# Kernel optimization log

Measured on AMD Instinct MI355X. Metric: run time of the kernel, lower is better.

The kernel has to match this reference:

```python
import jax, jax.numpy as jnp
import numpy as np

EPS = 1e-12  # F.normalize eps


def setup_inputs() -> dict:
    key = jax.random.key(0)
    ks = jax.random.split(key, 6)
    B, T, D = 8, 4096, 1024
    L, K, CD = 8, 1024, 16
    return {
        "z_e": jax.random.normal(ks[0], (B, T, D), jnp.float32),
        "Wd": jax.random.normal(ks[1], (L, CD, D), jnp.float32) * 0.02,
        "bd": jnp.zeros((L, CD), jnp.float32),
        "cb": jax.random.normal(ks[2], (L, K, CD), jnp.float32) * 0.02,
        "Wu": jax.random.normal(ks[3], (L, D, CD), jnp.float32) * 0.02,
        "bu": jnp.zeros((L, D), jnp.float32),
    }


def _l2norm(x):
    return x / jnp.maximum(jnp.linalg.norm(x, axis=-1, keepdims=True), EPS)


def reference(z_e, Wd, bd, cb, Wu, bu):
    """z_e: (B,T,D). Returns (z_q_concat, codes, commitment_loss, codebook_loss, entropy_loss)."""
    B, T, D = z_e.shape
    L, K, CD = cb.shape
    sg = jax.lax.stop_gradient
    residual = z_e
    zq_list, codes_list = [], []
    commit = jnp.asarray(0.0, z_e.dtype)
    cbl = jnp.asarray(0.0, z_e.dtype)
    for i in range(L):
        # proj_down: Linear(D -> CD), weight (CD, D)
        z_i = jnp.einsum('btd,cd->btc', residual, Wd[i]) + bd[i]  # (B,T,CD)
        flat = z_i.reshape(-1, CD)                                 # (N,CD)
        cb_i = cb[i]                                               # (K,CD)
        # L2-normalized lookup; argmin of euclidean cdist == argmin of squared dist
        zn, cbn = _l2norm(flat), _l2norm(cb_i)
        d2 = (jnp.sum(zn * zn, -1, keepdims=True)
              - 2.0 * (zn @ cbn.T)
              + jnp.sum(cbn * cbn, -1))                            # (N,K)
        codes = jnp.argmin(d2, axis=-1)                            # (N,)
        z_q = cb_i[codes].reshape(B, T, CD)                        # gather from RAW codebook
        commit = commit + jnp.mean((z_i - sg(z_q)) ** 2)
        cbl = cbl + jnp.mean((z_q - sg(z_i)) ** 2)
        zq_list.append(z_i + sg(z_q - z_i))                        # straight-through
        # residual update uses detached z_q; proj_up weight (D, CD)
        residual = residual - (jnp.einsum('btc,dc->btd', sg(z_q), Wu[i]) + bu[i])
        codes_list.append(codes.reshape(B, T))
    z_q_concat = jnp.concatenate(zq_list, axis=-1)                 # (B,T,L*CD)
    codes_all = jnp.stack(codes_list, axis=-1)                     # (B,T,L)
    entropy_loss = jnp.asarray(0.0, z_e.dtype)                     # entropy_loss_weight == 0
    return z_q_concat, codes_all, commit, cbl, entropy_loss
```

## Files before the change

### kernel.cpp

```cpp
#include <hip/hip_runtime.h>
#include <math.h>


#define TAU 3e-4f

#define WS_WACC   0
#define WS_HV64   64
#define WS_G64    2048
#define WS_CBN64  133120
#define WS_CBN32  1247232
#define WS_G32    1902592
#define WS_HV32   1968128
#define WS_BMAT   1968640
#define WS_SBU    2492928

__device__ __forceinline__ void gload_lds16(const void* g, void* l) {
    __builtin_amdgcn_global_load_lds(
        (const __attribute__((address_space(1))) void*)g,
        (__attribute__((address_space(3))) void*)l, 16, 0, 0);
}

__global__ void __launch_bounds__(256) rvq_prep1(
    const float* __restrict__ cb, const float* __restrict__ Wd,
    const float* __restrict__ bu,
    double* __restrict__ cbn64, float* __restrict__ cbn32,
    float* __restrict__ Bmat, double* __restrict__ sbu,
    double* __restrict__ wacc)
{
    const int b = blockIdx.x, t = threadIdx.x;
    if (b < 32) {
        const int idx = b * 256 + t;
        const float* cp = cb + (size_t)idx * 16;
        double v[16]; double n = 0.0;
#pragma unroll
        for (int c = 0; c < 16; ++c) { v[c] = (double)cp[c]; n = fma(v[c], v[c], n); }
        const double iv = 1.0 / fmax(sqrt(n), 1e-12);
        double* r64 = cbn64 + (size_t)idx * 17;
        float*  r32 = cbn32 + (size_t)idx * 20;
        double c2 = 0.0;
#pragma unroll
        for (int c = 0; c < 16; ++c) {
            const double x = v[c] * iv;
            c2 = fma(x, x, c2);
            r64[c] = x; r32[c] = (float)x;
        }
        r64[16] = c2;
        r32[16] = (float)c2; r32[17] = 0.f; r32[18] = 0.f; r32[19] = 0.f;
    } else if (b < 160) {
        const int ic = b - 32;
        const int d0 = t * 4;
        const float4 v = *(const float4*)(Wd + (size_t)ic * 1024 + d0);
        Bmat[(size_t)(d0 + 0) * 128 + ic] = v.x;
        Bmat[(size_t)(d0 + 1) * 128 + ic] = v.y;
        Bmat[(size_t)(d0 + 2) * 128 + ic] = v.z;
        Bmat[(size_t)(d0 + 3) * 128 + ic] = v.w;
    } else if (b < 192) {
        const int idx = b - 160;
        const int i = idx >> 2, d = (idx & 3) * 256 + t;
        double s = 0.0;
        for (int j = 0; j < i; ++j) s += (double)bu[j * 1024 + d];
        sbu[i * 1024 + d] = s;
    } else {
        if (t == 0) wacc[0] = 0.0;
    }
}

__global__ void __launch_bounds__(256) rvq_prep2(
    const float* __restrict__ Wu, const float* __restrict__ Wd,
    const float* __restrict__ bd, const double* __restrict__ sbu,
    double* __restrict__ G64, float* __restrict__ G32,
    double* __restrict__ hv64, float* __restrict__ hv32)
{
    __shared__ double sm2[1200];
    float* smf = (float*)sm2;
    const int b = blockIdx.x, t = threadIdx.x;
    if (b < 64) {
        const int j = b >> 3, i = b & 7;
        if (j >= i) return;
        float* Aus = smf;
        float* Bds = smf + 1280;
        const int a = t >> 4, bb = t & 15;
        double s = 0.0;
        for (int ch = 0; ch < 16; ++ch) {
            __syncthreads();
            {
                const int dd = t >> 2, a4 = (t & 3) * 4;
                const float4 v = *(const float4*)(Wu + (size_t)j * 16384
                                  + (size_t)(ch * 64 + dd) * 16 + a4);
                *(float4*)&Aus[dd * 20 + a4] = v;
                const int br = t >> 4, d4 = (t & 15) * 4;
                const float4 w = *(const float4*)(Wd + (size_t)i * 16384
                                  + (size_t)br * 1024 + ch * 64 + d4);
                *(float4*)&Bds[br * 68 + d4] = w;
            }
            __syncthreads();
#pragma unroll
            for (int dd = 0; dd < 64; ++dd)
                s = fma((double)Aus[dd * 20 + a], (double)Bds[bb * 68 + dd], s);
        }
        G64[(size_t)(j * 8 + i) * 256 + t] = s;
        G32[(size_t)(j * 8 + i) * 256 + t] = (float)s;
    } else {
        const int i = b - 64;
        const int dq = t >> 4, bb = t & 15;
        const double* sp = sbu + i * 1024 + dq * 64;
        const float*  wp = Wd + (size_t)i * 16384 + (size_t)bb * 1024 + dq * 64;
        double s = 0.0;
#pragma unroll
        for (int dd = 0; dd < 64; ++dd)
            s = fma(sp[dd], (double)wp[dd], s);
        sm2[dq * 20 + bb] = s;
        __syncthreads();
        if (t < 16) {
            double s2 = 0.0;
#pragma unroll
            for (int q = 0; q < 16; ++q) s2 += sm2[q * 20 + t];
            const double h = (double)bd[i * 16 + t] - s2;
            hv64[i * 16 + t] = h; hv32[i * 16 + t] = (float)h;
        }
    }
}

__global__ void __launch_bounds__(256, 4) rvq_main(
    const float* __restrict__ z_e, const float* __restrict__ Wd,
    const float* __restrict__ cb,
    const float* __restrict__ Bmat, const float* __restrict__ hv32,
    const double* __restrict__ hv64,
    const float* __restrict__ cbn32, const double* __restrict__ cbn64,
    const float* __restrict__ G32, const double* __restrict__ G64,
    double* __restrict__ wacc,
    float* __restrict__ out0, float* __restrict__ out1)
{
    __shared__ __attribute__((aligned(16))) double stag_d[1312];
    __shared__ float ybuf[32 * 132];
    __shared__ float znbuf[32 * 20];
    __shared__ float candd[128], candd2[128];
    __shared__ int   candk[128];
    __shared__ float zqs[32 * 17];
    __shared__ int   bkhist[256];
    __shared__ int   bks[32], flist[32];
    __shared__ int   flagcnt;
    float* stag = reinterpret_cast<float*>(stag_d);

    const int t = threadIdx.x;
    const int tok0g = blockIdx.x * 32;

    {
        float* As = stag;
        float* Bs = stag + 576;
        const int tg2 = t >> 5, cg2 = t & 31;
        const int wid = t >> 6, lane = t & 63;
        float acc[4][4];
#pragma unroll
        for (int h = 0; h < 4; ++h)
#pragma unroll
            for (int x = 0; x < 4; ++x) acc[h][x] = 0.f;

#pragma unroll 1
        for (int ko = 0; ko < 64; ++ko) {
            const int k0 = ko * 16;
            __syncthreads();
            {
                const int m = t >> 3, kk2 = (t & 7) * 2;
                const float2 v = *(const float2*)(z_e +
                    (size_t)(tok0g + m) * 1024 + k0 + kk2);
                As[kk2 * 36 + m] = v.x;
                As[(kk2 + 1) * 36 + m] = v.y;
            }
            {
                const float* bsrc = Bmat + (size_t)k0 * 128 + wid * 512 + lane * 4;
                float* bdst = Bs + wid * 512;
                gload_lds16(bsrc, bdst);
                gload_lds16(bsrc + 256, bdst + 256);
            }
            __syncthreads();
#pragma unroll
            for (int kk = 0; kk < 16; ++kk) {
                const float4 a4 = *(const float4*)&As[kk * 36 + tg2 * 4];
                const float4 b4 = *(const float4*)&Bs[kk * 128 + cg2 * 4];
                acc[0][0] = fmaf(a4.x, b4.x, acc[0][0]);
                acc[0][1] = fmaf(a4.x, b4.y, acc[0][1]);
                acc[0][2] = fmaf(a4.x, b4.z, acc[0][2]);
                acc[0][3] = fmaf(a4.x, b4.w, acc[0][3]);
                acc[1][0] = fmaf(a4.y, b4.x, acc[1][0]);
                acc[1][1] = fmaf(a4.y, b4.y, acc[1][1]);
                acc[1][2] = fmaf(a4.y, b4.z, acc[1][2]);
                acc[1][3] = fmaf(a4.y, b4.w, acc[1][3]);
                acc[2][0] = fmaf(a4.z, b4.x, acc[2][0]);
                acc[2][1] = fmaf(a4.z, b4.y, acc[2][1]);
                acc[2][2] = fmaf(a4.z, b4.z, acc[2][2]);
                acc[2][3] = fmaf(a4.z, b4.w, acc[2][3]);
                acc[3][0] = fmaf(a4.w, b4.x, acc[3][0]);
                acc[3][1] = fmaf(a4.w, b4.y, acc[3][1]);
                acc[3][2] = fmaf(a4.w, b4.z, acc[3][2]);
                acc[3][3] = fmaf(a4.w, b4.w, acc[3][3]);
            }
        }
        const float4 hv = *(const float4*)(hv32 + cg2 * 4);
#pragma unroll
        for (int h = 0; h < 4; ++h) {
            float4 y4;
            y4.x = acc[h][0] + hv.x;
            y4.y = acc[h][1] + hv.y;
            y4.z = acc[h][2] + hv.z;
            y4.w = acc[h][3] + hv.w;
            *(float4*)&ybuf[(tg2 * 4 + h) * 132 + cg2 * 4] = y4;
        }
    }

    double lacc = 0.0;
    const int cg = t >> 3, tg = t & 7;
#pragma unroll 1
    for (int l = 0; l < 8; ++l) {
        __syncthreads();
        if (t < 32) {
            const float* yr = &ybuf[t * 132 + l * 16];
            float yv[16]; float n2 = 0.f;
#pragma unroll
            for (int c = 0; c < 16; ++c) { yv[c] = yr[c]; n2 = fmaf(yv[c], yv[c], n2); }
            const float iv = 1.0f / fmaxf(sqrtf(n2), 1e-12f);
            float* zp = &znbuf[t * 20];
#pragma unroll
            for (int c = 0; c < 16; ++c) zp[c] = yv[c] * iv;
        }
        __syncthreads();

        float zn[4][16];
#pragma unroll
        for (int h = 0; h < 4; ++h) {
            const float* zp = &znbuf[(tg + 8 * h) * 20];
            const float4 z0 = *(const float4*)(zp);
            const float4 z1 = *(const float4*)(zp + 4);
            const float4 z2 = *(const float4*)(zp + 8);
            const float4 z3 = *(const float4*)(zp + 12);
            zn[h][0] = z0.x; zn[h][1] = z0.y; zn[h][2]  = z0.z; zn[h][3]  = z0.w;
            zn[h][4] = z1.x; zn[h][5] = z1.y; zn[h][6]  = z1.z; zn[h][7]  = z1.w;
            zn[h][8] = z2.x; zn[h][9] = z2.y; zn[h][10] = z2.z; zn[h][11] = z2.w;
            zn[h][12] = z3.x; zn[h][13] = z3.y; zn[h][14] = z3.z; zn[h][15] = z3.w;
        }

        float bs[4], bs2[4]; int bk[4];
#pragma unroll
        for (int h = 0; h < 4; ++h) { bs[h] = 1e30f; bs2[h] = 1e30f; bk[h] = -1; }
        const float* cb_l = cbn32 + (size_t)l * 1024 * 20;
#pragma unroll 2
        for (int kk = 0; kk < 32; ++kk) {
            const int k = (kk << 5) + cg;
            const float* rp = cb_l + (size_t)k * 20;
            const float4 c0 = *(const float4*)(rp);
            const float4 c1 = *(const float4*)(rp + 4);
            const float4 c2 = *(const float4*)(rp + 8);
            const float4 c3 = *(const float4*)(rp + 12);
            const float cn2 = rp[16];
#pragma unroll
            for (int h = 0; h < 4; ++h) {
                float d;
                d = c0.x * zn[h][0];
                d = fmaf(c0.y, zn[h][1], d);
                d = fmaf(c0.z, zn[h][2], d);
                d = fmaf(c0.w, zn[h][3], d);
                d = fmaf(c1.x, zn[h][4], d);
                d = fmaf(c1.y, zn[h][5], d);
                d = fmaf(c1.z, zn[h][6], d);
                d = fmaf(c1.w, zn[h][7], d);
                d = fmaf(c2.x, zn[h][8], d);
                d = fmaf(c2.y, zn[h][9], d);
                d = fmaf(c2.z, zn[h][10], d);
                d = fmaf(c2.w, zn[h][11], d);
                d = fmaf(c3.x, zn[h][12], d);
                d = fmaf(c3.y, zn[h][13], d);
                d = fmaf(c3.z, zn[h][14], d);
                d = fmaf(c3.w, zn[h][15], d);
                const float s = fmaf(-2.f, d, cn2);
                const bool w = s < bs[h];
                bs2[h] = w ? bs[h] : fminf(bs2[h], s);
                bk[h]  = w ? k : bk[h];
                bs[h]  = w ? s : bs[h];
            }
        }

#pragma unroll
        for (int m = 8; m <= 32; m <<= 1) {
#pragma unroll
            for (int h = 0; h < 4; ++h) {
                const float ob = __shfl_xor(bs[h], m);
                const float os = __shfl_xor(bs2[h], m);
                const int   ok = __shfl_xor(bk[h], m);
                const bool w = (ob < bs[h]) || (ob == bs[h] && ok < bk[h]);
                const float loser = w ? bs[h] : ob;
                bs2[h] = fminf(fminf(bs2[h], os), loser);
                bs[h]  = w ? ob : bs[h];
                bk[h]  = w ? ok : bk[h];
            }
        }
        if (t == 0) flagcnt = 0;
        if ((t & 63) < 8) {
            const int base = (t >> 6) * 32 + tg;
#pragma unroll
            for (int h = 0; h < 4; ++h) {
                candd [base + 8 * h] = bs[h];
                candd2[base + 8 * h] = bs2[h];
                candk [base + 8 * h] = bk[h];
            }
        }
        __syncthreads();
        if (t < 32) {
            float best = 1e30f, sec = 1e30f; int bkk = -1;
#pragma unroll
            for (int c = 0; c < 4; ++c) {
                const float d  = candd [c * 32 + t];
                const float d2 = candd2[c * 32 + t];
                const int   k  = candk [c * 32 + t];
                const bool w = (d < best) || (d == best && k < bkk);
                const float nw = fminf(sec, fminf(best, d2));
                const float nl = fminf(sec, d);
                sec  = w ? nw : nl;
                bkk  = w ? k : bkk;
                best = w ? d : best;
            }
            bks[t] = bkk;
            const float* yr = &ybuf[t * 132 + l * 16];
            float n2 = 0.f;
#pragma unroll
            for (int c = 0; c < 16; ++c) n2 = fmaf(yr[c], yr[c], n2);
            if ((sec - best < TAU) || (n2 < 1e-3f)) {
                const int p = atomicAdd(&flagcnt, 1); flist[p] = t;
            }
        }
        __syncthreads();

        const int nf = flagcnt;
#pragma unroll 1
        for (int f = 0; f < nf; ++f) {
            const int tok = flist[f];
            double* rpd = stag_d;
            {
                const int c = t & 15, ch = t >> 4;
                const float* gz = z_e + (size_t)(tok0g + tok) * 1024 + ch * 64;
                const float* wp = Wd + ((size_t)l * 16 + c) * 1024 + ch * 64;
                double pd = 0.0;
                for (int dd = 0; dd < 64; ++dd)
                    pd = fma((double)gz[dd], (double)wp[dd], pd);
                rpd[c * 16 + ch] = pd;
            }
            __syncthreads();
            if (t < 16) {
                double y = hv64[l * 16 + t];
#pragma unroll
                for (int ch = 0; ch < 16; ++ch) y += rpd[t * 16 + ch];
                for (int j = 0; j < l; ++j) {
                    const int bkj = bkhist[tok * 8 + j];
                    const float* qv = cb + ((size_t)j * 1024 + bkj) * 16;
                    const double* gp = G64 + (size_t)(j * 8 + l) * 256 + t;
                    double s = 0.0;
#pragma unroll
                    for (int a = 0; a < 16; ++a)
                        s = fma((double)qv[a], gp[a * 16], s);
                    y -= s;
                }
                rpd[256 + t] = y;
            }
            __syncthreads();
            if (t == 0) {
                double n2 = 0.0;
#pragma unroll
                for (int c = 0; c < 16; ++c) n2 = fma(rpd[256 + c], rpd[256 + c], n2);
                const double iv = 1.0 / fmax(sqrt(n2), 1e-12);
#pragma unroll
                for (int c = 0; c < 16; ++c) rpd[272 + c] = rpd[256 + c] * iv;
            }
            __syncthreads();
            {
                double bd_ = 1e300; int bk_ = -1;
#pragma unroll
                for (int q = 0; q < 4; ++q) {
                    const int k = q * 256 + t;
                    const double* row = cbn64 + (size_t)(l * 1024 + k) * 17;
                    double dot = 0.0;
#pragma unroll
                    for (int c = 0; c < 16; ++c) dot = fma(row[c], rpd[272 + c], dot);
                    const double s = fma(-2.0, dot, row[16]);
                    if (s < bd_) { bd_ = s; bk_ = k; }
                }
                rpd[288 + t] = bd_;
                ((int*)&rpd[544])[t] = bk_;
            }
            __syncthreads();
            if (t == 0) {
                double bd_ = 1e300; int bk_ = -1;
                for (int i = 0; i < 256; ++i) {
                    const double d = rpd[288 + i];
                    const int k = ((int*)&rpd[544])[i];
                    if (d < bd_ || (d == bd_ && k < bk_)) { bd_ = d; bk_ = k; }
                }
                bks[tok] = bk_;
            }
            __syncthreads();
        }

        if (t < 32) {
            const int bk_ = bks[t];
            bkhist[t * 8 + l] = bk_;
            const float4* qp = (const float4*)(cb + ((size_t)l * 1024 + bk_) * 16);
            const float4 q0 = qp[0], q1 = qp[1], q2 = qp[2], q3 = qp[3];
            float* op = out0 + (size_t)(tok0g + t) * 128 + l * 16;
            ((float4*)op)[0] = q0; ((float4*)op)[1] = q1;
            ((float4*)op)[2] = q2; ((float4*)op)[3] = q3;
            out1[(size_t)(tok0g + t) * 8 + l] = (float)bk_;
            const float qf[16] = {q0.x,q0.y,q0.z,q0.w, q1.x,q1.y,q1.z,q1.w,
                                  q2.x,q2.y,q2.z,q2.w, q3.x,q3.y,q3.z,q3.w};
#pragma unroll
            for (int a = 0; a < 16; ++a) zqs[t * 17 + a] = qf[a];
            const float* yr = &ybuf[t * 132 + l * 16];
#pragma unroll
            for (int c = 0; c < 16; ++c) {
                const float d = yr[c] - qf[c];
                lacc += (double)d * (double)d;
            }
        }
        __syncthreads();

        if (l < 7) {
            {
                const int total = (7 - l) * 256;
                for (int idx = t; idx < total; idx += 256) {
                    const int ii = l + 1 + (idx >> 8);
                    stag[idx] = G32[(size_t)(l * 8 + ii) * 256 + (idx & 255)];
                }
            }
            __syncthreads();
            const int part = t >> 5, tok = t & 31;
            const int ii = l + 1 + part;
            if (ii < 8) {
                float zql[16];
#pragma unroll
                for (int a = 0; a < 16; ++a) zql[a] = zqs[tok * 17 + a];
                const float* gb = &stag[part * 256];
                float corr[16];
#pragma unroll
                for (int x = 0; x < 16; ++x) corr[x] = 0.f;
#pragma unroll
                for (int a = 0; a < 16; ++a) {
                    const float4 g0 = *(const float4*)&gb[a * 16];
                    const float4 g1 = *(const float4*)&gb[a * 16 + 4];
                    const float4 g2 = *(const float4*)&gb[a * 16 + 8];
                    const float4 g3 = *(const float4*)&gb[a * 16 + 12];
                    const float za = zql[a];
                    corr[0]  = fmaf(za, g0.x, corr[0]);  corr[1]  = fmaf(za, g0.y, corr[1]);
                    corr[2]  = fmaf(za, g0.z, corr[2]);  corr[3]  = fmaf(za, g0.w, corr[3]);
                    corr[4]  = fmaf(za, g1.x, corr[4]);  corr[5]  = fmaf(za, g1.y, corr[5]);
                    corr[6]  = fmaf(za, g1.z, corr[6]);  corr[7]  = fmaf(za, g1.w, corr[7]);
                    corr[8]  = fmaf(za, g2.x, corr[8]);  corr[9]  = fmaf(za, g2.y, corr[9]);
                    corr[10] = fmaf(za, g2.z, corr[10]); corr[11] = fmaf(za, g2.w, corr[11]);
                    corr[12] = fmaf(za, g3.x, corr[12]); corr[13] = fmaf(za, g3.y, corr[13]);
                    corr[14] = fmaf(za, g3.z, corr[14]); corr[15] = fmaf(za, g3.w, corr[15]);
                }
                float* yr = &ybuf[tok * 132 + ii * 16];
#pragma unroll
                for (int v = 0; v < 4; ++v) {
                    float4 y4 = *(float4*)&yr[v * 4];
                    y4.x -= corr[v * 4 + 0]; y4.y -= corr[v * 4 + 1];
                    y4.z -= corr[v * 4 + 2]; y4.w -= corr[v * 4 + 3];
                    *(float4*)&yr[v * 4] = y4;
                }
            }
        }
    }

    if (t < 64) {
#pragma unroll
        for (int off = 32; off > 0; off >>= 1) lacc += __shfl_down(lacc, off);
        if (t == 0) atomicAdd(wacc, lacc);
    }
}

__global__ void __launch_bounds__(64) rvq_fin(const double* __restrict__ wacc,
                                              float* __restrict__ lossp) {
    if (threadIdx.x == 0) {
        const float v = (float)(wacc[0] * (1.0 / 524288.0));
        lossp[0] = v; lossp[1] = v; lossp[2] = 0.0f;
    }
}

extern "C" void kernel_launch(void* const* d_in, const int* in_sizes, int n_in,
                              void* d_out, int out_size, void* d_ws, size_t ws_size,
                              hipStream_t stream) {
    (void)in_sizes; (void)n_in; (void)ws_size;
    const float* z_e = (const float*)d_in[0];
    const float* Wd  = (const float*)d_in[1];
    const float* bd  = (const float*)d_in[2];
    const float* cb  = (const float*)d_in[3];
    const float* Wu  = (const float*)d_in[4];
    const float* bu  = (const float*)d_in[5];

    float* out0  = (float*)d_out;
    float* out1  = out0 + (size_t)8 * 4096 * 128;
    float* lossp = out0 + (size_t)out_size - 3;

    char* ws = (char*)d_ws;
    double* wacc  = (double*)(ws + WS_WACC);
    double* hv64  = (double*)(ws + WS_HV64);
    double* G64   = (double*)(ws + WS_G64);
    double* cbn64 = (double*)(ws + WS_CBN64);
    float*  cbn32 = (float*) (ws + WS_CBN32);
    float*  G32   = (float*) (ws + WS_G32);
    float*  hv32  = (float*) (ws + WS_HV32);
    float*  Bmat  = (float*) (ws + WS_BMAT);
    double* sbu   = (double*)(ws + WS_SBU);

    rvq_prep1<<<193, 256, 0, stream>>>(cb, Wd, bu, cbn64, cbn32, Bmat, sbu, wacc);
    rvq_prep2<<<72, 256, 0, stream>>>(Wu, Wd, bd, sbu, G64, G32, hv64, hv32);
    rvq_main<<<1024, 256, 0, stream>>>(z_e, Wd, cb, Bmat, hv32, hv64,
                                       cbn32, cbn64, G32, G64, wacc, out0, out1);
    rvq_fin<<<1, 64, 0, stream>>>(wacc, lossp);
}
```

Measured before the change: 685.1 us.

## Compute codebook distances with split-bf16 MFMA instead of scalar FP32 FMAs

Replaces the per-thread scalar FP32 dot-product search over the 1024 codebook entries with MFMA 16x16x32 bf16 instructions. Each operand is split into bf16 hi and lo parts, so the cross terms recover near-FP32 accuracy. The codebook is pre-split into bf16 hi/lo in the prep kernel, and the wave/lane mapping and candidate reduction are reorganized. The ‖c‖² term is dropped because the normalized codebook rows have unit norm. This relies on the existing ambiguity-tolerance fallback (TAU flagging with exact FP64 recheck) to absorb the extra rounding error.

```diff
diff --git a/kernel.cpp b/kernel.cpp
--- a/kernel.cpp
+++ b/kernel.cpp
@@ -8,22 +8,34 @@
 #define WS_HV64   64
 #define WS_G64    2048
 #define WS_CBN64  133120
-#define WS_CBN32  1247232
+#define WS_CBF    1247232
 #define WS_G32    1902592
 #define WS_HV32   1968128
 #define WS_BMAT   1968640
 #define WS_SBU    2492928
 
+typedef __attribute__((ext_vector_type(8))) short short8v;
+typedef __attribute__((ext_vector_type(4))) float f32x4;
+
 __device__ __forceinline__ void gload_lds16(const void* g, void* l) {
     __builtin_amdgcn_global_load_lds(
         (const __attribute__((address_space(1))) void*)g,
         (__attribute__((address_space(3))) void*)l, 16, 0, 0);
 }
 
+__device__ __forceinline__ unsigned short bf16_rne(float x) {
+    unsigned u = __float_as_uint(x);
+    u += 0x7FFFu + ((u >> 16) & 1u);
+    return (unsigned short)(u >> 16);
+}
+__device__ __forceinline__ float bf16_to_f32(unsigned short h) {
+    return __uint_as_float(((unsigned)h) << 16);
+}
+
 __global__ void __launch_bounds__(256) rvq_prep1(
     const float* __restrict__ cb, const float* __restrict__ Wd,
     const float* __restrict__ bu,
-    double* __restrict__ cbn64, float* __restrict__ cbn32,
+    double* __restrict__ cbn64, unsigned short* __restrict__ cbf,
     float* __restrict__ Bmat, double* __restrict__ sbu,
     double* __restrict__ wacc)
 {
@@ -36,16 +48,19 @@
         for (int c = 0; c < 16; ++c) { v[c] = (double)cp[c]; n = fma(v[c], v[c], n); }
         const double iv = 1.0 / fmax(sqrt(n), 1e-12);
         double* r64 = cbn64 + (size_t)idx * 17;
-        float*  r32 = cbn32 + (size_t)idx * 20;
+        unsigned short* cf = cbf + (size_t)idx * 32;
         double c2 = 0.0;
 #pragma unroll
         for (int c = 0; c < 16; ++c) {
             const double x = v[c] * iv;
             c2 = fma(x, x, c2);
-            r64[c] = x; r32[c] = (float)x;
+            r64[c] = x;
+            const float xf = (float)x;
+            const unsigned short hh = bf16_rne(xf);
+            cf[c] = hh;
+            cf[16 + c] = bf16_rne(xf - bf16_to_f32(hh));
         }
         r64[16] = c2;
-        r32[16] = (float)c2; r32[17] = 0.f; r32[18] = 0.f; r32[19] = 0.f;
     } else if (b < 160) {
         const int ic = b - 32;
         const int d0 = t * 4;
@@ -126,7 +141,7 @@
     const float* __restrict__ cb,
     const float* __restrict__ Bmat, const float* __restrict__ hv32,
     const double* __restrict__ hv64,
-    const float* __restrict__ cbn32, const double* __restrict__ cbn64,
+    const unsigned short* __restrict__ cbf, const double* __restrict__ cbn64,
     const float* __restrict__ G32, const double* __restrict__ G64,
     double* __restrict__ wacc,
     float* __restrict__ out0, float* __restrict__ out1)
@@ -134,8 +149,8 @@
     __shared__ __attribute__((aligned(16))) double stag_d[1312];
     __shared__ float ybuf[32 * 132];
     __shared__ float znbuf[32 * 20];
-    __shared__ float candd[128], candd2[128];
-    __shared__ int   candk[128];
+    __shared__ float candd[64], candd2[64];
+    __shared__ int   candk[64];
     __shared__ float zqs[32 * 17];
     __shared__ int   bkhist[256];
     __shared__ int   bks[32], flist[32];
@@ -209,7 +224,10 @@
     }
 
     double lacc = 0.0;
-    const int cg = t >> 3, tg = t & 7;
+    const int w = t >> 6, lane = t & 63;
+    const int blk = lane >> 4, col = lane & 15;
+    const int Tt = w & 1, Hh = w >> 1;
+    const bool lolane = blk >= 2;
 #pragma unroll 1
     for (int l = 0; l < 8; ++l) {
         __syncthreads();
@@ -225,98 +243,84 @@
         }
         __syncthreads();
 
-        float zn[4][16];
-#pragma unroll
-        for (int h = 0; h < 4; ++h) {
-            const float* zp = &znbuf[(tg + 8 * h) * 20];
-            const float4 z0 = *(const float4*)(zp);
+        short8v afrag;
+        {
+            const float* zp = &znbuf[(Tt * 16 + col) * 20 + (blk & 1) * 8];
+            const float4 z0 = *(const float4*)zp;
             const float4 z1 = *(const float4*)(zp + 4);
-            const float4 z2 = *(const float4*)(zp + 8);
-            const float4 z3 = *(const float4*)(zp + 12);
-            zn[h][0] = z0.x; zn[h][1] = z0.y; zn[h][2]  = z0.z; zn[h][3]  = z0.w;
-            zn[h][4] = z1.x; zn[h][5] = z1.y; zn[h][6]  = z1.z; zn[h][7]  = z1.w;
-            zn[h][8] = z2.x; zn[h][9] = z2.y; zn[h][10] = z2.z; zn[h][11] = z2.w;
-            zn[h][12] = z3.x; zn[h][13] = z3.y; zn[h][14] = z3.z; zn[h][15] = z3.w;
+            const float zv[8] = {z0.x, z0.y, z0.z, z0.w, z1.x, z1.y, z1.z, z1.w};
+#pragma unroll
+            for (int i = 0; i < 8; ++i) {
+                const float x = -2.f * zv[i];
+                const unsigned short h = bf16_rne(x);
+                const unsigned short v2 = lolane ? bf16_rne(x - bf16_to_f32(h)) : h;
+                afrag[i] = (short)v2;
+            }
         }
 
         float bs[4], bs2[4]; int bk[4];
 #pragma unroll
-        for (int h = 0; h < 4; ++h) { bs[h] = 1e30f; bs2[h] = 1e30f; bk[h] = -1; }
-        const float* cb_l = cbn32 + (size_t)l * 1024 * 20;
+        for (int r = 0; r < 4; ++r) { bs[r] = 1e30f; bs2[r] = 1e30f; bk[r] = -1; }
+        const unsigned short* cbp = cbf + ((size_t)(l * 1024 + Hh * 512 + col)) * 32;
+        const unsigned short* p1 = cbp + (blk & 1) * 8;
+        const unsigned short* p2 = cbp + 16 + (blk & 1) * 8;
 #pragma unroll 2
-        for (int kk = 0; kk < 32; ++kk) {
-            const int k = (kk << 5) + cg;
-            const float* rp = cb_l + (size_t)k * 20;
-            const float4 c0 = *(const float4*)(rp);
-            const float4 c1 = *(const float4*)(rp + 4);
-            const float4 c2 = *(const float4*)(rp + 8);
-            const float4 c3 = *(const float4*)(rp + 12);
-            const float cn2 = rp[16];
-#pragma unroll
-            for (int h = 0; h < 4; ++h) {
-                float d;
-                d = c0.x * zn[h][0];
-                d = fmaf(c0.y, zn[h][1], d);
-                d = fmaf(c0.z, zn[h][2], d);
-                d = fmaf(c0.w, zn[h][3], d);
-                d = fmaf(c1.x, zn[h][4], d);
-                d = fmaf(c1.y, zn[h][5], d);
-                d = fmaf(c1.z, zn[h][6], d);
-                d = fmaf(c1.w, zn[h][7], d);
-                d = fmaf(c2.x, zn[h][8], d);
-                d = fmaf(c2.y, zn[h][9], d);
-                d = fmaf(c2.z, zn[h][10], d);
-                d = fmaf(c2.w, zn[h][11], d);
-                d = fmaf(c3.x, zn[h][12], d);
-                d = fmaf(c3.y, zn[h][13], d);
-                d = fmaf(c3.z, zn[h][14], d);
-                d = fmaf(c3.w, zn[h][15], d);
-                const float s = fmaf(-2.f, d, cn2);
-                const bool w = s < bs[h];
-                bs2[h] = w ? bs[h] : fminf(bs2[h], s);
-                bk[h]  = w ? k : bk[h];
-                bs[h]  = w ? s : bs[h];
-            }
-        }
-
-#pragma unroll
-        for (int m = 8; m <= 32; m <<= 1) {
-#pragma unroll
-            for (int h = 0; h < 4; ++h) {
-                const float ob = __shfl_xor(bs[h], m);
-                const float os = __shfl_xor(bs2[h], m);
-                const int   ok = __shfl_xor(bk[h], m);
-                const bool w = (ob < bs[h]) || (ob == bs[h] && ok < bk[h]);
-                const float loser = w ? bs[h] : ob;
-                bs2[h] = fminf(fminf(bs2[h], os), loser);
-                bs[h]  = w ? ob : bs[h];
-                bk[h]  = w ? ok : bk[h];
+        for (int tile = 0; tile < 32; ++tile) {
+            const short8v b1 = *(const short8v*)(p1 + tile * 512);
+            short8v b2 = {};
+            if (!lolane) b2 = *(const short8v*)(p2 + tile * 512);
+            f32x4 acc = {0.f, 0.f, 0.f, 0.f};
+            acc = __builtin_amdgcn_mfma_f32_16x16x32_bf16(afrag, b1, acc, 0, 0, 0);
+            acc = __builtin_amdgcn_mfma_f32_16x16x32_bf16(afrag, b2, acc, 0, 0, 0);
+            const int k = Hh * 512 + tile * 16 + col;
+#pragma unroll
+            for (int r = 0; r < 4; ++r) {
+                const float s = acc[r];
+                const bool wn = s < bs[r];
+                bs2[r] = wn ? bs[r] : fminf(bs2[r], s);
+                bk[r]  = wn ? k : bk[r];
+                bs[r]  = wn ? s : bs[r];
+            }
+        }
+
+#pragma unroll
+        for (int m = 1; m <= 8; m <<= 1) {
+#pragma unroll
+            for (int r = 0; r < 4; ++r) {
+                const float ob = __shfl_xor(bs[r], m);
+                const float os = __shfl_xor(bs2[r], m);
+                const int   ok = __shfl_xor(bk[r], m);
+                const bool wn = (ob < bs[r]) || (ob == bs[r] && ok < bk[r]);
+                const float loser = wn ? bs[r] : ob;
+                bs2[r] = fminf(fminf(bs2[r], os), loser);
+                bs[r]  = wn ? ob : bs[r];
+                bk[r]  = wn ? ok : bk[r];
             }
         }
         if (t == 0) flagcnt = 0;
-        if ((t & 63) < 8) {
-            const int base = (t >> 6) * 32 + tg;
-#pragma unroll
-            for (int h = 0; h < 4; ++h) {
-                candd [base + 8 * h] = bs[h];
-                candd2[base + 8 * h] = bs2[h];
-                candk [base + 8 * h] = bk[h];
+        if (col == 0) {
+#pragma unroll
+            for (int r = 0; r < 4; ++r) {
+                const int tok = Tt * 16 + blk * 4 + r;
+                candd [Hh * 32 + tok] = bs[r];
+                candd2[Hh * 32 + tok] = bs2[r];
+                candk [Hh * 32 + tok] = bk[r];
             }
         }
         __syncthreads();
         if (t < 32) {
             float best = 1e30f, sec = 1e30f; int bkk = -1;
 #pragma unroll
-            for (int c = 0; c < 4; ++c) {
+            for (int c = 0; c < 2; ++c) {
                 const float d  = candd [c * 32 + t];
                 const float d2 = candd2[c * 32 + t];
                 const int   k  = candk [c * 32 + t];
-                const bool w = (d < best) || (d == best && k < bkk);
+                const bool wn = (d < best) || (d == best && k < bkk);
                 const float nw = fminf(sec, fminf(best, d2));
                 const float nl = fminf(sec, d);
-                sec  = w ? nw : nl;
-                bkk  = w ? k : bkk;
-                best = w ? d : best;
+                sec  = wn ? nw : nl;
+                bkk  = wn ? k : bkk;
+                best = wn ? d : best;
             }
             bks[t] = bkk;
             const float* yr = &ybuf[t * 132 + l * 16];
@@ -502,15 +506,15 @@
     double* hv64  = (double*)(ws + WS_HV64);
     double* G64   = (double*)(ws + WS_G64);
     double* cbn64 = (double*)(ws + WS_CBN64);
-    float*  cbn32 = (float*) (ws + WS_CBN32);
+    unsigned short* cbf = (unsigned short*)(ws + WS_CBF);
     float*  G32   = (float*) (ws + WS_G32);
     float*  hv32  = (float*) (ws + WS_HV32);
     float*  Bmat  = (float*) (ws + WS_BMAT);
     double* sbu   = (double*)(ws + WS_SBU);
 
-    rvq_prep1<<<193, 256, 0, stream>>>(cb, Wd, bu, cbn64, cbn32, Bmat, sbu, wacc);
+    rvq_prep1<<<193, 256, 0, stream>>>(cb, Wd, bu, cbn64, cbf, Bmat, sbu, wacc);
     rvq_prep2<<<72, 256, 0, stream>>>(Wu, Wd, bd, sbu, G64, G32, hv64, hv32);
     rvq_main<<<1024, 256, 0, stream>>>(z_e, Wd, cb, Bmat, hv32, hv64,
-                                       cbn32, cbn64, G32, G64, wacc, out0, out1);
+                                       cbf, cbn64, G32, G64, wacc, out0, out1);
     rvq_fin<<<1, 64, 0, stream>>>(wacc, lossp);
 }
```

Result: faster. 658.2 us (-3.9%).
